# Optimization experiments

Measured on AMD Instinct MI355X. Metric: run time of the kernel, lower is better.

## Reference

```python
import jax, jax.numpy as jnp
import numpy as np

B, TE, TD, H = 8, 512, 256, 256  # batch, enc len, dec len, hidden (He==Hd)

def setup_inputs() -> dict:
    key = jax.random.key(0)
    k1, k2, k3, k4, k5 = jax.random.split(key, 5)
    # Keras 'uniform' initializer: U(-0.05, 0.05)
    u = lambda k, s: jax.random.uniform(k, s, jnp.float32, -0.05, 0.05)
    return {
        "encoder_out_seq": jax.random.normal(k1, (B, TE, H), jnp.float32),
        "decoder_out_seq": jax.random.normal(k2, (B, TD, H), jnp.float32),
        "W_a": u(k3, (H, H)),
        "U_a": u(k4, (H, H)),
        "V_a": u(k5, (H, 1)),
    }

def reference(encoder_out_seq, decoder_out_seq, W_a, U_a, V_a):
    # Bahdanau additive attention, fully batched (same math as the per-step K.rnn loop)
    We = jnp.einsum('bih,hk->bik', encoder_out_seq, W_a)   # [B,Te,H]
    Uh = jnp.einsum('bjh,hk->bjk', decoder_out_seq, U_a)   # [B,Td,H]
    # energies: V_a^T tanh(We_i + Uh_j)  -> [B,Td,Te]
    t = jnp.tanh(We[:, None, :, :] + Uh[:, :, None, :])    # [B,Td,Te,H]
    e = jnp.einsum('bjih,h->bji', t, V_a[:, 0])             # [B,Td,Te]
    e = jax.nn.softmax(e, axis=-1)                          # softmax over encoder positions
    c = jnp.einsum('bji,bih->bjh', e, encoder_out_seq)      # [B,Td,H]
    return (c, e)
```

## Files before the change

### kernel.cpp

```cpp
#include <hip/hip_runtime.h>


#define BB 8
#define TE 512
#define TD 256
#define HH 256

#define EXP2F(x) __builtin_amdgcn_exp2f(x)
#define RCPF(x)  __builtin_amdgcn_rcpf(x)
#define KSCALE   2.8853900817779268f
#define NSC      (-2.8853900817779268f)

__global__ __launch_bounds__(256) void k_pre(
    const float* __restrict__ enc, const float* __restrict__ dec,
    const float* __restrict__ Wa,  const float* __restrict__ Ua,
    float* __restrict__ W4, float* __restrict__ Uhe)
{
    const int tid = threadIdx.x;
    const bool is_enc = blockIdx.x < 256;
    const int bi = is_enc ? blockIdx.x : (blockIdx.x - 256);
    const int m0 = (bi >> 2) * 64;
    const int n0 = (bi & 3) * 64;
    const float* X = is_enc ? enc : dec;
    const float* W = is_enc ? Wa : Ua;

    __shared__ float Xs[32][68];
    __shared__ float Ws[32][68];

    const int kq = tid & 7,  xr = tid >> 3;
    const int wk = tid >> 3, wn = (tid & 7) * 8;
    const int tx = tid & 15, ty = tid >> 4;

    float acc[4][4];
    #pragma unroll
    for (int r = 0; r < 4; r++)
        #pragma unroll
        for (int c = 0; c < 4; c++) acc[r][c] = 0.f;

    for (int kc = 0; kc < HH; kc += 32) {
        float4 xa = *(const float4*)(X + (size_t)(m0 + xr) * HH + kc + kq * 4);
        float4 xb = *(const float4*)(X + (size_t)(m0 + xr + 32) * HH + kc + kq * 4);
        float4 wa = *(const float4*)(W + (size_t)(kc + wk) * HH + n0 + wn);
        float4 wb = *(const float4*)(W + (size_t)(kc + wk) * HH + n0 + wn + 4);
        __syncthreads();
        Xs[kq * 4 + 0][xr] = xa.x; Xs[kq * 4 + 1][xr] = xa.y;
        Xs[kq * 4 + 2][xr] = xa.z; Xs[kq * 4 + 3][xr] = xa.w;
        Xs[kq * 4 + 0][xr + 32] = xb.x; Xs[kq * 4 + 1][xr + 32] = xb.y;
        Xs[kq * 4 + 2][xr + 32] = xb.z; Xs[kq * 4 + 3][xr + 32] = xb.w;
        *(float4*)&Ws[wk][wn]     = wa;
        *(float4*)&Ws[wk][wn + 4] = wb;
        __syncthreads();
        #pragma unroll
        for (int k = 0; k < 32; k++) {
            float4 a = *(const float4*)&Xs[k][ty * 4];
            float4 b = *(const float4*)&Ws[k][tx * 4];
            acc[0][0] = fmaf(a.x, b.x, acc[0][0]); acc[0][1] = fmaf(a.x, b.y, acc[0][1]);
            acc[0][2] = fmaf(a.x, b.z, acc[0][2]); acc[0][3] = fmaf(a.x, b.w, acc[0][3]);
            acc[1][0] = fmaf(a.y, b.x, acc[1][0]); acc[1][1] = fmaf(a.y, b.y, acc[1][1]);
            acc[1][2] = fmaf(a.y, b.z, acc[1][2]); acc[1][3] = fmaf(a.y, b.w, acc[1][3]);
            acc[2][0] = fmaf(a.z, b.x, acc[2][0]); acc[2][1] = fmaf(a.z, b.y, acc[2][1]);
            acc[2][2] = fmaf(a.z, b.z, acc[2][2]); acc[2][3] = fmaf(a.z, b.w, acc[2][3]);
            acc[3][0] = fmaf(a.w, b.x, acc[3][0]); acc[3][1] = fmaf(a.w, b.y, acc[3][1]);
            acc[3][2] = fmaf(a.w, b.z, acc[3][2]); acc[3][3] = fmaf(a.w, b.w, acc[3][3]);
        }
    }

    if (is_enc) {
        const int b  = m0 >> 9;
        const int ib = (m0 & 511) + ty * 4;
        const int hq = (n0 >> 2) + tx;
        float* dst = W4 + (((size_t)b * 64 + hq) * TE + ib) * 4;
        #pragma unroll
        for (int r = 0; r < 4; r++) {
            float4 v;
            v.x = EXP2F(acc[r][0] * KSCALE); v.y = EXP2F(acc[r][1] * KSCALE);
            v.z = EXP2F(acc[r][2] * KSCALE); v.w = EXP2F(acc[r][3] * KSCALE);
            *(float4*)(dst + (size_t)r * 4) = v;
        }
    } else {
        #pragma unroll
        for (int r = 0; r < 4; r++) {
            float4 v;
            v.x = EXP2F(acc[r][0] * KSCALE); v.y = EXP2F(acc[r][1] * KSCALE);
            v.z = EXP2F(acc[r][2] * KSCALE); v.w = EXP2F(acc[r][3] * KSCALE);
            *(float4*)(Uhe + (size_t)(m0 + ty * 4 + r) * HH + n0 + tx * 4) = v;
        }
    }
}

__global__ __launch_bounds__(512) void k_attn(
    const float* __restrict__ enc, const float* __restrict__ W4,
    const float* __restrict__ Uhe, const float* __restrict__ Va,
    float* __restrict__ out_c, float* __restrict__ out_e)
{
    const int wv = threadIdx.x >> 6, lane = threadIdx.x & 63;
    const int b   = blockIdx.x >> 7;
    const int j0  = (blockIdx.x & 127) * 2;
    const int jj0 = b * TD + j0;

    __shared__ float sP[TE][2];
    __shared__ float sR[8][2][HH];

    const int i = (wv << 6) + lane;
    const float* wp = W4 + ((size_t)b * 64 * TE + i) * 4;
    const float* ua = Uhe + (size_t)jj0 * HH;
    const float* va = Va;

    float a0 = 0.f, a1 = 0.f;
    #pragma unroll 2
    for (int q = 0; q < 64; q++) {
        float4 w4 = *(const float4*)(wp + (size_t)q * TE * 4);
        float4 v4 = *(const float4*)(va + 4 * q);
        float4 u0 = *(const float4*)(ua + 4 * q);
        float4 u1 = *(const float4*)(ua + HH + 4 * q);
        a0 = fmaf(v4.x, RCPF(fmaf(w4.x, u0.x, 1.f)), a0);
        a0 = fmaf(v4.y, RCPF(fmaf(w4.y, u0.y, 1.f)), a0);
        a0 = fmaf(v4.z, RCPF(fmaf(w4.z, u0.z, 1.f)), a0);
        a0 = fmaf(v4.w, RCPF(fmaf(w4.w, u0.w, 1.f)), a0);
        a1 = fmaf(v4.x, RCPF(fmaf(w4.x, u1.x, 1.f)), a1);
        a1 = fmaf(v4.y, RCPF(fmaf(w4.y, u1.y, 1.f)), a1);
        a1 = fmaf(v4.z, RCPF(fmaf(w4.z, u1.z, 1.f)), a1);
        a1 = fmaf(v4.w, RCPF(fmaf(w4.w, u1.w, 1.f)), a1);
    }
    float2 E; E.x = NSC * a0; E.y = NSC * a1;
    *(float2*)&sP[i][0] = E;
    __syncthreads();

    if (wv < 2) {
        float ev[8];
        float m = -3.0e38f;
        #pragma unroll
        for (int k = 0; k < 8; k++) {
            ev[k] = sP[lane + 64 * k][wv];
            m = fmaxf(m, ev[k]);
        }
        #pragma unroll
        for (int off = 32; off; off >>= 1) m = fmaxf(m, __shfl_xor(m, off, 64));
        float s = 0.f;
        #pragma unroll
        for (int k = 0; k < 8; k++) { ev[k] = EXP2F(ev[k] - m); s += ev[k]; }
        #pragma unroll
        for (int off = 32; off; off >>= 1) s += __shfl_xor(s, off, 64);
        float rs = RCPF(s);
        float* oe = out_e + (size_t)(jj0 + wv) * TE;
        #pragma unroll
        for (int k = 0; k < 8; k++) {
            float p = ev[k] * rs;
            sP[lane + 64 * k][wv] = p;
            oe[lane + 64 * k] = p;
        }
    }
    __syncthreads();

    const int ib = wv << 6;
    const float* eb = enc + ((size_t)b * TE + ib) * HH + 4 * lane;
    float4 c0 = {0,0,0,0}, c1 = {0,0,0,0};
    #pragma unroll 2
    for (int k = 0; k < 64; k++) {
        float2 p = *(const float2*)&sP[ib + k][0];
        float4 q = *(const float4*)(eb + (size_t)k * HH);
        c0.x = fmaf(p.x, q.x, c0.x); c0.y = fmaf(p.x, q.y, c0.y);
        c0.z = fmaf(p.x, q.z, c0.z); c0.w = fmaf(p.x, q.w, c0.w);
        c1.x = fmaf(p.y, q.x, c1.x); c1.y = fmaf(p.y, q.y, c1.y);
        c1.z = fmaf(p.y, q.z, c1.z); c1.w = fmaf(p.y, q.w, c1.w);
    }
    *(float4*)&sR[wv][0][4 * lane] = c0;
    *(float4*)&sR[wv][1][4 * lane] = c1;
    __syncthreads();

    {
        const int jr = wv & 1;
        const int h  = (wv >> 1) * 64 + lane;
        float s = 0.f;
        #pragma unroll
        for (int ww = 0; ww < 8; ww++) s += sR[ww][jr][h];
        out_c[(size_t)(jj0 + jr) * HH + h] = s;
    }
}

extern "C" void kernel_launch(void* const* d_in, const int* in_sizes, int n_in,
                              void* d_out, int out_size, void* d_ws, size_t ws_size,
                              hipStream_t stream) {
    const float* enc = (const float*)d_in[0];
    const float* dec = (const float*)d_in[1];
    const float* Wa  = (const float*)d_in[2];
    const float* Ua  = (const float*)d_in[3];
    const float* Va  = (const float*)d_in[4];

    float* W4  = (float*)d_ws;
    float* Uhe = W4 + (size_t)BB * HH * TE;

    float* out_c = (float*)d_out;
    float* out_e = out_c + (size_t)BB * TD * HH;

    k_pre<<<384, 256, 0, stream>>>(enc, dec, Wa, Ua, W4, Uhe);
    k_attn<<<BB * TD / 2, 512, 0, stream>>>(enc, W4, Uhe, Va, out_c, out_e);
}
```

Measured before the change: 126.2 us.

## Process four decoder rows per attention block and interleave batches across blocks

Each attention block now handles four decoder positions instead of two. Each W4 load and each encoder-row load is reused across four accumulators, halving global traffic per output, and the grid is halved to 512 blocks. Block indexing now puts the batch index in the low bits, so consecutive blocks work on different batches. The cost is more registers, a larger shared-memory reduction buffer (about 40KB), and fewer blocks for occupancy.

```diff
diff --git a/kernel.cpp b/kernel.cpp
--- a/kernel.cpp
+++ b/kernel.cpp
@@ -94,25 +94,27 @@
     float* __restrict__ out_c, float* __restrict__ out_e)
 {
     const int wv = threadIdx.x >> 6, lane = threadIdx.x & 63;
-    const int b   = blockIdx.x >> 7;
-    const int j0  = (blockIdx.x & 127) * 2;
+    const int b   = blockIdx.x & 7;
+    const int j0  = (blockIdx.x >> 3) * 4;
     const int jj0 = b * TD + j0;
 
-    __shared__ float sP[TE][2];
-    __shared__ float sR[8][2][HH];
+    __shared__ float sP[4][TE];
+    __shared__ float sR[8][4][HH];
 
     const int i = (wv << 6) + lane;
     const float* wp = W4 + ((size_t)b * 64 * TE + i) * 4;
     const float* ua = Uhe + (size_t)jj0 * HH;
     const float* va = Va;
 
-    float a0 = 0.f, a1 = 0.f;
+    float a0 = 0.f, a1 = 0.f, a2 = 0.f, a3 = 0.f;
     #pragma unroll 2
     for (int q = 0; q < 64; q++) {
         float4 w4 = *(const float4*)(wp + (size_t)q * TE * 4);
         float4 v4 = *(const float4*)(va + 4 * q);
         float4 u0 = *(const float4*)(ua + 4 * q);
         float4 u1 = *(const float4*)(ua + HH + 4 * q);
+        float4 u2 = *(const float4*)(ua + 2 * HH + 4 * q);
+        float4 u3 = *(const float4*)(ua + 3 * HH + 4 * q);
         a0 = fmaf(v4.x, RCPF(fmaf(w4.x, u0.x, 1.f)), a0);
         a0 = fmaf(v4.y, RCPF(fmaf(w4.y, u0.y, 1.f)), a0);
         a0 = fmaf(v4.z, RCPF(fmaf(w4.z, u0.z, 1.f)), a0);
@@ -121,17 +123,27 @@
         a1 = fmaf(v4.y, RCPF(fmaf(w4.y, u1.y, 1.f)), a1);
         a1 = fmaf(v4.z, RCPF(fmaf(w4.z, u1.z, 1.f)), a1);
         a1 = fmaf(v4.w, RCPF(fmaf(w4.w, u1.w, 1.f)), a1);
-    }
-    float2 E; E.x = NSC * a0; E.y = NSC * a1;
-    *(float2*)&sP[i][0] = E;
+        a2 = fmaf(v4.x, RCPF(fmaf(w4.x, u2.x, 1.f)), a2);
+        a2 = fmaf(v4.y, RCPF(fmaf(w4.y, u2.y, 1.f)), a2);
+        a2 = fmaf(v4.z, RCPF(fmaf(w4.z, u2.z, 1.f)), a2);
+        a2 = fmaf(v4.w, RCPF(fmaf(w4.w, u2.w, 1.f)), a2);
+        a3 = fmaf(v4.x, RCPF(fmaf(w4.x, u3.x, 1.f)), a3);
+        a3 = fmaf(v4.y, RCPF(fmaf(w4.y, u3.y, 1.f)), a3);
+        a3 = fmaf(v4.z, RCPF(fmaf(w4.z, u3.z, 1.f)), a3);
+        a3 = fmaf(v4.w, RCPF(fmaf(w4.w, u3.w, 1.f)), a3);
+    }
+    sP[0][i] = NSC * a0;
+    sP[1][i] = NSC * a1;
+    sP[2][i] = NSC * a2;
+    sP[3][i] = NSC * a3;
     __syncthreads();
 
-    if (wv < 2) {
+    if (wv < 4) {
         float ev[8];
         float m = -3.0e38f;
         #pragma unroll
         for (int k = 0; k < 8; k++) {
-            ev[k] = sP[lane + 64 * k][wv];
+            ev[k] = sP[wv][lane + 64 * k];
             m = fmaxf(m, ev[k]);
         }
         #pragma unroll
@@ -146,7 +158,7 @@
         #pragma unroll
         for (int k = 0; k < 8; k++) {
             float p = ev[k] * rs;
-            sP[lane + 64 * k][wv] = p;
+            sP[wv][lane + 64 * k] = p;
             oe[lane + 64 * k] = p;
         }
     }
@@ -154,27 +166,40 @@
 
     const int ib = wv << 6;
     const float* eb = enc + ((size_t)b * TE + ib) * HH + 4 * lane;
-    float4 c0 = {0,0,0,0}, c1 = {0,0,0,0};
+    float4 c0 = {0,0,0,0}, c1 = {0,0,0,0}, c2 = {0,0,0,0}, c3 = {0,0,0,0};
     #pragma unroll 2
     for (int k = 0; k < 64; k++) {
-        float2 p = *(const float2*)&sP[ib + k][0];
+        float p0 = sP[0][ib + k];
+        float p1 = sP[1][ib + k];
+        float p2 = sP[2][ib + k];
+        float p3 = sP[3][ib + k];
         float4 q = *(const float4*)(eb + (size_t)k * HH);
-        c0.x = fmaf(p.x, q.x, c0.x); c0.y = fmaf(p.x, q.y, c0.y);
-        c0.z = fmaf(p.x, q.z, c0.z); c0.w = fmaf(p.x, q.w, c0.w);
-        c1.x = fmaf(p.y, q.x, c1.x); c1.y = fmaf(p.y, q.y, c1.y);
-        c1.z = fmaf(p.y, q.z, c1.z); c1.w = fmaf(p.y, q.w, c1.w);
+        c0.x = fmaf(p0, q.x, c0.x); c0.y = fmaf(p0, q.y, c0.y);
+        c0.z = fmaf(p0, q.z, c0.z); c0.w = fmaf(p0, q.w, c0.w);
+        c1.x = fmaf(p1, q.x, c1.x); c1.y = fmaf(p1, q.y, c1.y);
+        c1.z = fmaf(p1, q.z, c1.z); c1.w = fmaf(p1, q.w, c1.w);
+        c2.x = fmaf(p2, q.x, c2.x); c2.y = fmaf(p2, q.y, c2.y);
+        c2.z = fmaf(p2, q.z, c2.z); c2.w = fmaf(p2, q.w, c2.w);
+        c3.x = fmaf(p3, q.x, c3.x); c3.y = fmaf(p3, q.y, c3.y);
+        c3.z = fmaf(p3, q.z, c3.z); c3.w = fmaf(p3, q.w, c3.w);
     }
     *(float4*)&sR[wv][0][4 * lane] = c0;
     *(float4*)&sR[wv][1][4 * lane] = c1;
+    *(float4*)&sR[wv][2][4 * lane] = c2;
+    *(float4*)&sR[wv][3][4 * lane] = c3;
     __syncthreads();
 
     {
-        const int jr = wv & 1;
-        const int h  = (wv >> 1) * 64 + lane;
-        float s = 0.f;
-        #pragma unroll
-        for (int ww = 0; ww < 8; ww++) s += sR[ww][jr][h];
-        out_c[(size_t)(jj0 + jr) * HH + h] = s;
+        const int jr = wv & 3;
+        const int h2 = (wv >> 2) * 128 + 2 * lane;
+        float sx = 0.f, sy = 0.f;
+        #pragma unroll
+        for (int ww = 0; ww < 8; ww++) {
+            float2 t = *(const float2*)&sR[ww][jr][h2];
+            sx += t.x; sy += t.y;
+        }
+        float2 o; o.x = sx; o.y = sy;
+        *(float2*)(out_c + (size_t)(jj0 + jr) * HH + h2) = o;
     }
 }
 
@@ -194,5 +219,5 @@
     float* out_e = out_c + (size_t)BB * TD * HH;
 
     k_pre<<<384, 256, 0, stream>>>(enc, dec, Wa, Ua, W4, Uhe);
-    k_attn<<<BB * TD / 2, 512, 0, stream>>>(enc, W4, Uhe, Va, out_c, out_e);
+    k_attn<<<BB * TD / 4, 512, 0, stream>>>(enc, W4, Uhe, Va, out_c, out_e);
 }
```

Measured after the change: 120.0 us. 1.05x faster.

## Combine four reciprocals into one and use packed v2f math for energy loop

Applied to the files above, without the earlier changes.

The energy loop now sums v/(1+wu) terms four at a time over a common denominator, so it issues one reciprocal per group of four instead of four. It uses packed two-wide FMAs over an interleaved Uhe layout that pairs the two decoder rows. The context accumulation is also done with packed v2f FMAs, block-to-batch mapping is interleaved across batches, and launch bounds ask for higher occupancy. This trades transcendental throughput for extra multiplies and risks overflow or precision loss in the product of four exponential-based denominators.

```diff
diff --git a/kernel.cpp b/kernel.cpp
--- a/kernel.cpp
+++ b/kernel.cpp
@@ -11,10 +11,12 @@
 #define KSCALE   2.8853900817779268f
 #define NSC      (-2.8853900817779268f)
 
+typedef float v2f __attribute__((ext_vector_type(2)));
+
 __global__ __launch_bounds__(256) void k_pre(
     const float* __restrict__ enc, const float* __restrict__ dec,
     const float* __restrict__ Wa,  const float* __restrict__ Ua,
-    float* __restrict__ W4, float* __restrict__ Uhe)
+    float* __restrict__ W4, float* __restrict__ Uhe2)
 {
     const int tid = threadIdx.x;
     const bool is_enc = blockIdx.x < 256;
@@ -80,22 +82,24 @@
     } else {
         #pragma unroll
         for (int r = 0; r < 4; r++) {
-            float4 v;
-            v.x = EXP2F(acc[r][0] * KSCALE); v.y = EXP2F(acc[r][1] * KSCALE);
-            v.z = EXP2F(acc[r][2] * KSCALE); v.w = EXP2F(acc[r][3] * KSCALE);
-            *(float4*)(Uhe + (size_t)(m0 + ty * 4 + r) * HH + n0 + tx * 4) = v;
+            const int j = m0 + ty * 4 + r;
+            float* dst = Uhe2 + ((size_t)(j >> 1) * HH + n0 + tx * 4) * 2 + (j & 1);
+            dst[0] = EXP2F(acc[r][0] * KSCALE);
+            dst[2] = EXP2F(acc[r][1] * KSCALE);
+            dst[4] = EXP2F(acc[r][2] * KSCALE);
+            dst[6] = EXP2F(acc[r][3] * KSCALE);
         }
     }
 }
 
-__global__ __launch_bounds__(512) void k_attn(
+__global__ __launch_bounds__(512, 8) void k_attn(
     const float* __restrict__ enc, const float* __restrict__ W4,
-    const float* __restrict__ Uhe, const float* __restrict__ Va,
+    const float* __restrict__ Uhe2, const float* __restrict__ Va,
     float* __restrict__ out_c, float* __restrict__ out_e)
 {
     const int wv = threadIdx.x >> 6, lane = threadIdx.x & 63;
-    const int b   = blockIdx.x >> 7;
-    const int j0  = (blockIdx.x & 127) * 2;
+    const int b   = blockIdx.x & 7;
+    const int j0  = (blockIdx.x >> 3) * 2;
     const int jj0 = b * TD + j0;
 
     __shared__ float sP[TE][2];
@@ -103,26 +107,36 @@
 
     const int i = (wv << 6) + lane;
     const float* wp = W4 + ((size_t)b * 64 * TE + i) * 4;
-    const float* ua = Uhe + (size_t)jj0 * HH;
-    const float* va = Va;
-
-    float a0 = 0.f, a1 = 0.f;
-    #pragma unroll 2
+    const float4* up = (const float4*)(Uhe2 + (size_t)(jj0 >> 1) * HH * 2);
+    const float4* vp = (const float4*)Va;
+
+    v2f acc = {0.f, 0.f};
+    const v2f one = {1.f, 1.f};
+
+    #pragma unroll 4
     for (int q = 0; q < 64; q++) {
         float4 w4 = *(const float4*)(wp + (size_t)q * TE * 4);
-        float4 v4 = *(const float4*)(va + 4 * q);
-        float4 u0 = *(const float4*)(ua + 4 * q);
-        float4 u1 = *(const float4*)(ua + HH + 4 * q);
-        a0 = fmaf(v4.x, RCPF(fmaf(w4.x, u0.x, 1.f)), a0);
-        a0 = fmaf(v4.y, RCPF(fmaf(w4.y, u0.y, 1.f)), a0);
-        a0 = fmaf(v4.z, RCPF(fmaf(w4.z, u0.z, 1.f)), a0);
-        a0 = fmaf(v4.w, RCPF(fmaf(w4.w, u0.w, 1.f)), a0);
-        a1 = fmaf(v4.x, RCPF(fmaf(w4.x, u1.x, 1.f)), a1);
-        a1 = fmaf(v4.y, RCPF(fmaf(w4.y, u1.y, 1.f)), a1);
-        a1 = fmaf(v4.z, RCPF(fmaf(w4.z, u1.z, 1.f)), a1);
-        a1 = fmaf(v4.w, RCPF(fmaf(w4.w, u1.w, 1.f)), a1);
-    }
-    float2 E; E.x = NSC * a0; E.y = NSC * a1;
+        float4 v4  = vp[q];
+        float4 u01 = up[2 * q];
+        float4 u23 = up[2 * q + 1];
+        v2f uA; uA.x = u01.x; uA.y = u01.y;
+        v2f uB; uB.x = u01.z; uB.y = u01.w;
+        v2f uC; uC.x = u23.x; uC.y = u23.y;
+        v2f uD; uD.x = u23.z; uD.y = u23.w;
+        v2f A = __builtin_elementwise_fma((v2f)(w4.x), uA, one);
+        v2f B = __builtin_elementwise_fma((v2f)(w4.y), uB, one);
+        v2f C = __builtin_elementwise_fma((v2f)(w4.z), uC, one);
+        v2f D = __builtin_elementwise_fma((v2f)(w4.w), uD, one);
+        v2f dAB = A * B, dCD = C * D;
+        v2f nAB = __builtin_elementwise_fma((v2f)(v4.x), B, (v2f)(v4.y) * A);
+        v2f nCD = __builtin_elementwise_fma((v2f)(v4.z), D, (v2f)(v4.w) * C);
+        v2f num = __builtin_elementwise_fma(nAB, dCD, nCD * dAB);
+        v2f den = dAB * dCD;
+        v2f r; r.x = RCPF(den.x); r.y = RCPF(den.y);
+        acc = __builtin_elementwise_fma(num, r, acc);
+    }
+
+    float2 E; E.x = NSC * acc.x; E.y = NSC * acc.y;
     *(float2*)&sP[i][0] = E;
     __syncthreads();
 
@@ -154,18 +168,23 @@
 
     const int ib = wv << 6;
     const float* eb = enc + ((size_t)b * TE + ib) * HH + 4 * lane;
-    float4 c0 = {0,0,0,0}, c1 = {0,0,0,0};
+    v2f cx = {0,0}, cy = {0,0}, cz = {0,0}, cw = {0,0};
     #pragma unroll 2
     for (int k = 0; k < 64; k++) {
-        float2 p = *(const float2*)&sP[ib + k][0];
+        float2 pr = *(const float2*)&sP[ib + k][0];
+        v2f p; p.x = pr.x; p.y = pr.y;
         float4 q = *(const float4*)(eb + (size_t)k * HH);
-        c0.x = fmaf(p.x, q.x, c0.x); c0.y = fmaf(p.x, q.y, c0.y);
-        c0.z = fmaf(p.x, q.z, c0.z); c0.w = fmaf(p.x, q.w, c0.w);
-        c1.x = fmaf(p.y, q.x, c1.x); c1.y = fmaf(p.y, q.y, c1.y);
-        c1.z = fmaf(p.y, q.z, c1.z); c1.w = fmaf(p.y, q.w, c1.w);
-    }
-    *(float4*)&sR[wv][0][4 * lane] = c0;
-    *(float4*)&sR[wv][1][4 * lane] = c1;
+        cx = __builtin_elementwise_fma(p, (v2f)(q.x), cx);
+        cy = __builtin_elementwise_fma(p, (v2f)(q.y), cy);
+        cz = __builtin_elementwise_fma(p, (v2f)(q.z), cz);
+        cw = __builtin_elementwise_fma(p, (v2f)(q.w), cw);
+    }
+    {
+        float4 c0; c0.x = cx.x; c0.y = cy.x; c0.z = cz.x; c0.w = cw.x;
+        float4 c1; c1.x = cx.y; c1.y = cy.y; c1.z = cz.y; c1.w = cw.y;
+        *(float4*)&sR[wv][0][4 * lane] = c0;
+        *(float4*)&sR[wv][1][4 * lane] = c1;
+    }
     __syncthreads();
 
     {
@@ -187,12 +206,12 @@
     const float* Ua  = (const float*)d_in[3];
     const float* Va  = (const float*)d_in[4];
 
-    float* W4  = (float*)d_ws;
-    float* Uhe = W4 + (size_t)BB * HH * TE;
+    float* W4   = (float*)d_ws;
+    float* Uhe2 = W4 + (size_t)BB * HH * TE;
 
     float* out_c = (float*)d_out;
     float* out_e = out_c + (size_t)BB * TD * HH;
 
-    k_pre<<<384, 256, 0, stream>>>(enc, dec, Wa, Ua, W4, Uhe);
-    k_attn<<<BB * TD / 2, 512, 0, stream>>>(enc, W4, Uhe, Va, out_c, out_e);
+    k_pre<<<384, 256, 0, stream>>>(enc, dec, Wa, Ua, W4, Uhe2);
+    k_attn<<<BB * TD / 2, 512, 0, stream>>>(enc, W4, Uhe2, Va, out_c, out_e);
 }
```

Result: no change. 124.2 us (-1.5%).
